# Kernel optimization log

Hardware: AMD Instinct MI355X
Metric: run time of the kernel (lower is better)

The kernel has to match this reference:

```python
import jax, jax.numpy as jnp
import numpy as np

DIM = 1536      # model dim
NH = 12         # num heads
HD = 128        # head dim
F, H, W = 3, 26, 48   # video latent grid (frames, height, width)
S = F * H * W   # sequence length = 3744
B = 1
EPS = 1e-6
C2 = HD // 2    # 64 rotary pairs per head
SPLITS = [C2 - 2 * (C2 // 3), C2 // 3, C2 // 3]  # [22, 21, 21] for (f, h, w)


def _rope_angles():
    """Wan rope_params: concat of per-axis inverse-frequency angle tables, [1024, 64]."""
    def rp(dim):  # returns [1024, dim//2]
        inv = 1.0 / (10000.0 ** (np.arange(0, dim, 2, dtype=np.float64) / dim))
        return np.outer(np.arange(1024, dtype=np.float64), inv)
    a = np.concatenate([rp(HD - 4 * (HD // 6)), rp(2 * (HD // 6)), rp(2 * (HD // 6))], axis=1)
    return jnp.asarray(a, jnp.float32)


def setup_inputs() -> dict:
    key = jax.random.key(0)
    ks = jax.random.split(key, 9)
    std = DIM ** -0.5
    return {
        "x": jax.random.normal(ks[0], (B, S, DIM), jnp.float32),
        "wq": jax.random.normal(ks[1], (DIM, DIM), jnp.float32) * std,
        "bq": jnp.zeros((DIM,), jnp.float32),
        "wk": jax.random.normal(ks[2], (DIM, DIM), jnp.float32) * std,
        "bk": jnp.zeros((DIM,), jnp.float32),
        "wv": jax.random.normal(ks[3], (DIM, DIM), jnp.float32) * std,
        "bv": jnp.zeros((DIM,), jnp.float32),
        "wo": jax.random.normal(ks[4], (DIM, DIM), jnp.float32) * std,
        "bo": jnp.zeros((DIM,), jnp.float32),
        "gq": jnp.ones((DIM,), jnp.float32),   # WanRMSNorm weight for q
        "gk": jnp.ones((DIM,), jnp.float32),   # WanRMSNorm weight for k
        "freqs": _rope_angles(),                # [1024, 64] rotary angles
        "seq_lens": jnp.full((B,), S, jnp.int32),
    }


def _rmsnorm(y, g):
    return y * jax.lax.rsqrt(jnp.mean(jnp.square(y), axis=-1, keepdims=True) + EPS) * g


def _rope_grid(freqs):
    """Build per-position rotary angles [S, C2] from the 3D grid (F,H,W)."""
    af = freqs[:F, :SPLITS[0]]                       # [F, 22]
    ah = freqs[:H, SPLITS[0]:SPLITS[0] + SPLITS[1]]  # [H, 21]
    aw = freqs[:W, SPLITS[0] + SPLITS[1]:]           # [W, 21]
    ang = jnp.concatenate([
        jnp.broadcast_to(af[:, None, None, :], (F, H, W, SPLITS[0])),
        jnp.broadcast_to(ah[None, :, None, :], (F, H, W, SPLITS[1])),
        jnp.broadcast_to(aw[None, None, :, :], (F, H, W, SPLITS[2])),
    ], axis=-1)
    return ang.reshape(S, C2)


def _rope_apply(t, cos, sin):
    # t: [B, S, NH, HD]; pairs (even, odd) rotated by angle.
    tp = t.reshape(B, S, NH, C2, 2)
    xr, xi = tp[..., 0], tp[..., 1]
    yr = xr * cos - xi * sin
    yi = xr * sin + xi * cos
    return jnp.stack([yr, yi], axis=-1).reshape(B, S, NH, HD)


def reference(x, wq, bq, wk, bk, wv, bv, wo, bo, gq, gk, freqs, seq_lens):
    q = _rmsnorm(x @ wq.T + bq, gq).reshape(B, S, NH, HD)
    k = _rmsnorm(x @ wk.T + bk, gk).reshape(B, S, NH, HD)
    v = (x @ wv.T + bv).reshape(B, S, NH, HD)

    ang = _rope_grid(freqs)                    # [S, C2]
    cos = jnp.cos(ang)[None, :, None, :]       # [1, S, 1, C2]
    sin = jnp.sin(ang)[None, :, None, :]
    q = _rope_apply(q, cos, sin)
    k = _rope_apply(k, cos, sin)

    scale = HD ** -0.5
    scores = jnp.einsum('bqhd,bkhd->bhqk', q, k) * scale   # [B, NH, S, S]
    kmask = jnp.arange(S)[None, :] < seq_lens[:, None]     # [B, S]
    scores = jnp.where(kmask[:, None, None, :], scores, jnp.float32(-1e9))
    attn = jax.nn.softmax(scores, axis=-1)
    out = jnp.einsum('bhqk,bkhd->bqhd', attn, v).reshape(B, S, DIM)
    return out @ wo.T + bo
```

## Files before the change

### kernel.cpp

```cpp
#include <hip/hip_runtime.h>
#include <stdint.h>


#define DIM   1536
#define S_TOT 3744
#define NHEAD 12
#define HD    128

using short8 = __attribute__((ext_vector_type(8))) short;
using f32x4  = __attribute__((ext_vector_type(4))) float;
using f32x2  = __attribute__((ext_vector_type(2))) float;

__device__ __forceinline__ unsigned short f2bf(float f) {
  unsigned u = __builtin_bit_cast(unsigned, f);
  u += 0x7fffu + ((u >> 16) & 1u);
  return (unsigned short)(u >> 16);
}

__device__ __forceinline__ void gl_lds16(const void* g, void* l) {
  auto gp = (const __attribute__((address_space(1))) unsigned int*)g;
  auto lp = (__attribute__((address_space(3))) unsigned int*)(uintptr_t)l;
  __builtin_amdgcn_global_load_lds(gp, lp, 16, 0, 0);
}

#define NX4 (S_TOT * DIM / 4)
#define NW4 (DIM * DIM / 4)
__global__ __launch_bounds__(256) void cvt5_kernel(
    const float* __restrict__ x, const float* __restrict__ wq,
    const float* __restrict__ wk, const float* __restrict__ wv,
    const float* __restrict__ wo,
    unsigned short* __restrict__ xb, unsigned short* __restrict__ wqb,
    unsigned short* __restrict__ wkb, unsigned short* __restrict__ wvb,
    unsigned short* __restrict__ wob) {
  int gid = blockIdx.x * 256 + threadIdx.x;
  const float* src; unsigned short* dst; int off;
  if (gid < NX4)                { src = x;  dst = xb;  off = gid; }
  else if (gid < NX4 + NW4)     { src = wq; dst = wqb; off = gid - NX4; }
  else if (gid < NX4 + 2 * NW4) { src = wk; dst = wkb; off = gid - NX4 - NW4; }
  else if (gid < NX4 + 3 * NW4) { src = wv; dst = wvb; off = gid - NX4 - 2 * NW4; }
  else if (gid < NX4 + 4 * NW4) { src = wo; dst = wob; off = gid - NX4 - 3 * NW4; }
  else return;
  float4 v = ((const float4*)src)[off];
  ushort4 o;
  o.x = f2bf(v.x); o.y = f2bf(v.y); o.z = f2bf(v.z); o.w = f2bf(v.w);
  ((ushort4*)dst)[off] = o;
}

__device__ __forceinline__ void gemm_body(const unsigned short* __restrict__ A,
                                          const unsigned short* __restrict__ W,
                                          const float* __restrict__ bias,
                                          float* __restrict__ outF,
                                          unsigned short* __restrict__ outB,
                                          int M, int mode) {
  constexpr int K = DIM, N = DIM;
  __shared__ unsigned short As[128 * 32];
  __shared__ unsigned short Ws[128 * 32];
  int tid = threadIdx.x;
  int w = tid >> 6, lane = tid & 63;
  int wr = w >> 1, wc = w & 1, q4 = lane >> 4, ql = lane & 15;
  int m0 = blockIdx.y * 128, n0 = blockIdx.x * 128;

  f32x4 acc[4][4];
  const f32x4 zero4 = {0.f, 0.f, 0.f, 0.f};
#pragma unroll
  for (int i = 0; i < 4; i++)
#pragma unroll
    for (int j = 0; j < 4; j++) acc[i][j] = zero4;

  for (int k0 = 0; k0 < K; k0 += 32) {
    __syncthreads();
#pragma unroll
    for (int r = 0; r < 2; r++) {
      int idx = r * 256 + tid;
      int row = idx >> 2, ch = idx & 3;
      int am = m0 + row; am = (am < M) ? am : (M - 1);
      gl_lds16(A + (size_t)am * K + k0 + ch * 8, &As[idx * 8]);
      gl_lds16(W + (size_t)(n0 + row) * K + k0 + ch * 8, &Ws[idx * 8]);
    }
    __syncthreads();
    short8 af[4], wf[4];
#pragma unroll
    for (int i = 0; i < 4; i++)
      af[i] = *(const short8*)&As[(wr * 64 + i * 16 + ql) * 32 + q4 * 8];
#pragma unroll
    for (int j = 0; j < 4; j++)
      wf[j] = *(const short8*)&Ws[(wc * 64 + j * 16 + ql) * 32 + q4 * 8];
#pragma unroll
    for (int i = 0; i < 4; i++)
#pragma unroll
      for (int j = 0; j < 4; j++)
        acc[i][j] = __builtin_amdgcn_mfma_f32_16x16x32_bf16(af[i], wf[j], acc[i][j], 0, 0, 0);
  }

  float bb[4];
#pragma unroll
  for (int j = 0; j < 4; j++) bb[j] = bias[n0 + wc * 64 + j * 16 + ql];
#pragma unroll
  for (int i = 0; i < 4; i++) {
#pragma unroll
    for (int rg = 0; rg < 4; rg++) {
      int row = m0 + wr * 64 + i * 16 + q4 * 4 + rg;
      if (row < M) {
#pragma unroll
        for (int j = 0; j < 4; j++) {
          int col = n0 + wc * 64 + j * 16 + ql;
          float v = acc[i][j][rg] + bb[j];
          if (mode == 0) outF[(size_t)row * N + col] = v;
          else           outB[(size_t)row * N + col] = f2bf(v);
        }
      }
    }
  }
}

__global__ __launch_bounds__(256) void gemm_qkv_kernel(
    const unsigned short* __restrict__ xb,
    const unsigned short* __restrict__ wqb, const unsigned short* __restrict__ wkb,
    const unsigned short* __restrict__ wvb,
    const float* __restrict__ bq, const float* __restrict__ bk, const float* __restrict__ bv,
    float* __restrict__ Yq, float* __restrict__ Yk, unsigned short* __restrict__ Vb) {
  int z = blockIdx.z;
  const unsigned short* W = (z == 0) ? wqb : ((z == 1) ? wkb : wvb);
  const float* bias       = (z == 0) ? bq  : ((z == 1) ? bk  : bv);
  float* outF             = (z == 0) ? Yq  : Yk;
  gemm_body(xb, W, bias, outF, Vb, S_TOT, (z == 2) ? 1 : 0);
}

__global__ __launch_bounds__(256) void gemm_out_kernel(
    const unsigned short* __restrict__ AO, const unsigned short* __restrict__ wob,
    const float* __restrict__ bo, float* __restrict__ out) {
  gemm_body(AO, wob, bo, out, nullptr, S_TOT, 0);
}

__global__ __launch_bounds__(256) void normrope_kernel(
    const float* __restrict__ Yq, const float* __restrict__ Yk,
    const float* __restrict__ gq, const float* __restrict__ gk,
    const float* __restrict__ freqs,
    unsigned short* __restrict__ Qb, unsigned short* __restrict__ Kb) {
  int s = blockIdx.x;
  int tid = threadIdx.x;
  int w = tid >> 6, lane = tid & 63;
  const f32x2* yq2 = (const f32x2*)(Yq + (size_t)s * DIM);
  const f32x2* yk2 = (const f32x2*)(Yk + (size_t)s * DIM);
  f32x2 vq[3], vk[3];
  float ssq = 0.f, ssk = 0.f;
#pragma unroll
  for (int r = 0; r < 3; r++) {
    int p = tid + 256 * r;
    vq[r] = yq2[p]; vk[r] = yk2[p];
    ssq += vq[r].x * vq[r].x + vq[r].y * vq[r].y;
    ssk += vk[r].x * vk[r].x + vk[r].y * vk[r].y;
  }
#pragma unroll
  for (int d = 1; d < 64; d <<= 1) {
    ssq += __shfl_xor(ssq, d);
    ssk += __shfl_xor(ssk, d);
  }
  __shared__ float rq[4], rk[4];
  if (lane == 0) { rq[w] = ssq; rk[w] = ssk; }
  __syncthreads();
  float tq = rq[0] + rq[1] + rq[2] + rq[3];
  float tk = rk[0] + rk[1] + rk[2] + rk[3];
  float invq = rsqrtf(tq * (1.f / DIM) + 1e-6f);
  float invk = rsqrtf(tk * (1.f / DIM) + 1e-6f);

  int fi = s / (26 * 48);
  int hi = (s / 48) % 26;
  int wi = s % 48;
#pragma unroll
  for (int r = 0; r < 3; r++) {
    int p = tid + 256 * r;
    int c = p & 63;
    int frow = (c < 22) ? fi : ((c < 43) ? hi : wi);
    float ang = freqs[frow * 64 + c];
    float sn, cs;
    __sincosf(ang, &sn, &cs);
    {
      float a = vq[r].x * invq * gq[2 * p];
      float b = vq[r].y * invq * gq[2 * p + 1];
      ushort2 o; o.x = f2bf(a * cs - b * sn); o.y = f2bf(a * sn + b * cs);
      ((ushort2*)Qb)[(size_t)s * (DIM / 2) + p] = o;
    }
    {
      float a = vk[r].x * invk * gk[2 * p];
      float b = vk[r].y * invk * gk[2 * p + 1];
      ushort2 o; o.x = f2bf(a * cs - b * sn); o.y = f2bf(a * sn + b * cs);
      ((ushort2*)Kb)[(size_t)s * (DIM / 2) + p] = o;
    }
  }
}

__global__ __launch_bounds__(256) void vtrans_kernel(const unsigned short* __restrict__ Vb,
                                                     unsigned short* __restrict__ Vt) {
  int d0 = blockIdx.x * 64, s0 = blockIdx.y * 64;
  __shared__ unsigned short t[64][65];
  int tid = threadIdx.x;
#pragma unroll
  for (int r = 0; r < 4; r++) {
    int idx = r * 256 + tid;
    int sr = idx >> 4, c4 = (idx & 15) * 4;
    ushort4 v; v.x = v.y = v.z = v.w = 0;
    int s = s0 + sr;
    if (s < S_TOT) v = *(const ushort4*)(Vb + (size_t)s * DIM + d0 + c4);
    t[sr][c4 + 0] = v.x; t[sr][c4 + 1] = v.y; t[sr][c4 + 2] = v.z; t[sr][c4 + 3] = v.w;
  }
  __syncthreads();
#pragma unroll
  for (int r = 0; r < 4; r++) {
    int idx = r * 256 + tid;
    int dr = idx >> 4, s4 = (idx & 15) * 4;
    if (s0 + s4 < S_TOT) {
      ushort4 v;
      v.x = t[s4 + 0][dr]; v.y = t[s4 + 1][dr]; v.z = t[s4 + 2][dr]; v.w = t[s4 + 3][dr];
      *(ushort4*)(Vt + (size_t)(d0 + dr) * S_TOT + s0 + s4) = v;
    }
  }
}

__global__ __launch_bounds__(128, 2) void attn_kernel(
    const unsigned short* __restrict__ Qb, const unsigned short* __restrict__ Kb,
    const unsigned short* __restrict__ Vt, unsigned short* __restrict__ AO,
    const int* __restrict__ seq_lens) {
  int h = blockIdx.y;
  int tid = threadIdx.x;
  int w = tid >> 6, lane = tid & 63;
  int q4 = lane >> 4, ql = lane & 15;
  int seqlen = seq_lens[0]; if (seqlen > S_TOT) seqlen = S_TOT;

  __shared__ unsigned short Kl[64 * 128];
  __shared__ unsigned short Vl[128 * 64];
  __shared__ unsigned short Pl[2][32 * 72];
  __shared__ float stat[2][32];

  int q0 = blockIdx.x * 64 + w * 32;
  bool wact = (q0 < S_TOT);

  short8 qf[2][4];
#pragma unroll
  for (int qh = 0; qh < 2; qh++) {
    int qrow = q0 + qh * 16 + ql; if (qrow > S_TOT - 1) qrow = S_TOT - 1;
#pragma unroll
    for (int ks = 0; ks < 4; ks++)
      qf[qh][ks] = *(const short8*)(Qb + (size_t)qrow * DIM + h * HD + ks * 32 + q4 * 8);
  }

  f32x4 o[2][8];
  const f32x4 zero4 = {0.f, 0.f, 0.f, 0.f};
#pragma unroll
  for (int qh = 0; qh < 2; qh++)
#pragma unroll
    for (int nt = 0; nt < 8; nt++) o[qh][nt] = zero4;
  float m_run[2] = {-3.0e38f, -3.0e38f}, l_run[2] = {0.f, 0.f};
  const float sm_scale = 0.08838834764831845f;

  const size_t hoff = (size_t)h * HD;

  for (int kt = 0; kt < (S_TOT + 63) / 64; kt++) {
    int k0 = kt * 64;
    __syncthreads();
    {
      const unsigned short* kseg = Kb + (size_t)k0 * DIM + hoff;
#pragma unroll
      for (int r = 0; r < 8; r++) {
        int idx = r * 128 + tid;
        int row = idx >> 4, c = idx & 15;
        int g = c ^ (row & 15);
        gl_lds16(kseg + (size_t)row * DIM + g * 8, &Kl[idx * 8]);
      }
      int kmax = S_TOT - 8 - k0;
#pragma unroll
      for (int r = 0; r < 8; r++) {
        int idx = r * 128 + tid;
        int row = idx >> 3, c = idx & 7;
        int g = c ^ (row & 7);
        int kc = g * 8; if (kc > kmax) kc = kmax;
        gl_lds16(Vt + (hoff + row) * S_TOT + k0 + kc, &Vl[idx * 8]);
      }
    }
    __syncthreads();
    if (!wact) continue;

    f32x4 st[4][2];
#pragma unroll
    for (int mt = 0; mt < 4; mt++) {
      st[mt][0] = zero4; st[mt][1] = zero4;
#pragma unroll
      for (int ks = 0; ks < 4; ks++) {
        int c = (ks * 4 + q4) ^ ql;
        short8 kf = *(const short8*)&Kl[(mt * 16 + ql) * 128 + c * 8];
        st[mt][0] = __builtin_amdgcn_mfma_f32_16x16x32_bf16(kf, qf[0][ks], st[mt][0], 0, 0, 0);
        st[mt][1] = __builtin_amdgcn_mfma_f32_16x16x32_bf16(kf, qf[1][ks], st[mt][1], 0, 0, 0);
      }
    }

#pragma unroll
    for (int qh = 0; qh < 2; qh++) {
      float sc[16];
      float mloc = -3.0e38f;
#pragma unroll
      for (int mt = 0; mt < 4; mt++)
#pragma unroll
        for (int rg = 0; rg < 4; rg++) {
          int key = k0 + mt * 16 + q4 * 4 + rg;
          float v = st[mt][qh][rg] * sm_scale;
          v = (key < seqlen) ? v : -3.0e38f;
          sc[mt * 4 + rg] = v;
          mloc = fmaxf(mloc, v);
        }
      mloc = fmaxf(mloc, __shfl_xor(mloc, 16));
      mloc = fmaxf(mloc, __shfl_xor(mloc, 32));
      float mnew = fmaxf(m_run[qh], mloc);
      float alpha = __expf(m_run[qh] - mnew);
      m_run[qh] = mnew;
      float lloc = 0.f;
#pragma unroll
      for (int mt = 0; mt < 4; mt++) {
        ushort4 pk;
        float p0 = (k0 + mt * 16 + q4 * 4 + 0 < seqlen) ? __expf(sc[mt * 4 + 0] - mnew) : 0.f;
        float p1 = (k0 + mt * 16 + q4 * 4 + 1 < seqlen) ? __expf(sc[mt * 4 + 1] - mnew) : 0.f;
        float p2 = (k0 + mt * 16 + q4 * 4 + 2 < seqlen) ? __expf(sc[mt * 4 + 2] - mnew) : 0.f;
        float p3 = (k0 + mt * 16 + q4 * 4 + 3 < seqlen) ? __expf(sc[mt * 4 + 3] - mnew) : 0.f;
        lloc += p0 + p1 + p2 + p3;
        pk.x = f2bf(p0); pk.y = f2bf(p1); pk.z = f2bf(p2); pk.w = f2bf(p3);
        *(ushort4*)&Pl[w][(qh * 16 + ql) * 72 + mt * 16 + q4 * 4] = pk;
      }
      lloc += __shfl_xor(lloc, 16);
      lloc += __shfl_xor(lloc, 32);
      l_run[qh] = l_run[qh] * alpha + lloc;
      if (lane < 16) stat[w][qh * 16 + lane] = alpha;
    }

    float ar[2][4];
#pragma unroll
    for (int qh = 0; qh < 2; qh++)
#pragma unroll
      for (int rg = 0; rg < 4; rg++) ar[qh][rg] = stat[w][qh * 16 + q4 * 4 + rg];
#pragma unroll
    for (int qh = 0; qh < 2; qh++)
#pragma unroll
      for (int nt = 0; nt < 8; nt++)
#pragma unroll
        for (int rg = 0; rg < 4; rg++) o[qh][nt][rg] *= ar[qh][rg];

#pragma unroll
    for (int ks2 = 0; ks2 < 2; ks2++) {
      short8 pa0 = *(const short8*)&Pl[w][(0 * 16 + ql) * 72 + ks2 * 32 + q4 * 8];
      short8 pa1 = *(const short8*)&Pl[w][(1 * 16 + ql) * 72 + ks2 * 32 + q4 * 8];
#pragma unroll
      for (int nt = 0; nt < 8; nt++) {
        int c = (ks2 * 4 + q4) ^ (ql & 7);
        short8 vb = *(const short8*)&Vl[(nt * 16 + ql) * 64 + c * 8];
        o[0][nt] = __builtin_amdgcn_mfma_f32_16x16x32_bf16(pa0, vb, o[0][nt], 0, 0, 0);
        o[1][nt] = __builtin_amdgcn_mfma_f32_16x16x32_bf16(pa1, vb, o[1][nt], 0, 0, 0);
      }
    }
  }

  if (wact) {
    if (lane < 16) {
      stat[w][lane]      = 1.0f / l_run[0];
      stat[w][16 + lane] = 1.0f / l_run[1];
    }
#pragma unroll
    for (int qh = 0; qh < 2; qh++) {
#pragma unroll
      for (int rg = 0; rg < 4; rg++) {
        int row = q0 + qh * 16 + q4 * 4 + rg;
        if (row < S_TOT) {
          float il = stat[w][qh * 16 + q4 * 4 + rg];
#pragma unroll
          for (int nt = 0; nt < 8; nt++)
            AO[(size_t)row * DIM + h * HD + nt * 16 + ql] = f2bf(o[qh][nt][rg] * il);
        }
      }
    }
  }
}

extern "C" void kernel_launch(void* const* d_in, const int* in_sizes, int n_in,
                              void* d_out, int out_size, void* d_ws, size_t ws_size,
                              hipStream_t stream) {
  const float* x    = (const float*)d_in[0];
  const float* wq   = (const float*)d_in[1];
  const float* bq   = (const float*)d_in[2];
  const float* wk   = (const float*)d_in[3];
  const float* bk   = (const float*)d_in[4];
  const float* wv   = (const float*)d_in[5];
  const float* bv   = (const float*)d_in[6];
  const float* wo   = (const float*)d_in[7];
  const float* bo   = (const float*)d_in[8];
  const float* gq   = (const float*)d_in[9];
  const float* gk   = (const float*)d_in[10];
  const float* freqs = (const float*)d_in[11];
  const int*   seq  = (const int*)d_in[12];

  char* ws = (char*)d_ws;
  const size_t SZ_X = (size_t)S_TOT * DIM * 2;
  const size_t SZ_W = (size_t)DIM * DIM * 2;
  const size_t SZ_Y = (size_t)S_TOT * DIM * 4;

  unsigned short* xb  = (unsigned short*)(ws);
  unsigned short* wqb = (unsigned short*)(ws + SZ_X);
  unsigned short* wkb = (unsigned short*)(ws + SZ_X + SZ_W);
  unsigned short* wvb = (unsigned short*)(ws + SZ_X + 2 * SZ_W);
  unsigned short* wob = (unsigned short*)(ws + SZ_X + 3 * SZ_W);
  float*          Yq  = (float*)(ws + SZ_X + 4 * SZ_W);
  float*          Yk  = (float*)(ws + SZ_X + 4 * SZ_W + SZ_Y);
  unsigned short* Vb  = (unsigned short*)(ws + SZ_X + 4 * SZ_W + 2 * SZ_Y);
  unsigned short* Qb  = (unsigned short*)(ws + SZ_X + 4 * SZ_W + 2 * SZ_Y + SZ_X);
  unsigned short* Kb  = (unsigned short*)(ws + SZ_X + 4 * SZ_W + 2 * SZ_Y + 2 * SZ_X);
  unsigned short* Vt  = (unsigned short*)(ws + SZ_X + 4 * SZ_W + 2 * SZ_Y + 3 * SZ_X);
  unsigned short* AO  = (unsigned short*)(ws + SZ_X + 4 * SZ_W + 2 * SZ_Y + 4 * SZ_X);

  int total4 = NX4 + 4 * NW4;
  cvt5_kernel<<<dim3((total4 + 255) / 256), 256, 0, stream>>>(
      x, wq, wk, wv, wo, xb, wqb, wkb, wvb, wob);

  gemm_qkv_kernel<<<dim3(DIM / 128, (S_TOT + 127) / 128, 3), 256, 0, stream>>>(
      xb, wqb, wkb, wvb, bq, bk, bv, Yq, Yk, Vb);

  normrope_kernel<<<dim3(S_TOT), 256, 0, stream>>>(Yq, Yk, gq, gk, freqs, Qb, Kb);

  vtrans_kernel<<<dim3(DIM / 64, (S_TOT + 63) / 64), 256, 0, stream>>>(Vb, Vt);

  attn_kernel<<<dim3((S_TOT + 63) / 64, NHEAD), 128, 0, stream>>>(Qb, Kb, Vt, AO, seq);

  gemm_out_kernel<<<dim3(DIM / 128, (S_TOT + 127) / 128), 256, 0, stream>>>(
      AO, wob, bo, (float*)d_out);
}
```

Baseline: 477.5 us.

## Load K/V fragments directly from global memory in single-wave attention blocks

The attention kernel drops the shared-memory staging of K and V tiles and the block-wide barriers. Each 64-thread block now handles 32 queries and reads MFMA operands straight from global memory (relying on L2/L1 for reuse). The softmax scale is folded into Q during norm/rope, and the masking branch is split into unmasked full tiles and masked tail tiles via a template. The alpha and 1/l broadcasts now use shuffles instead of LDS. The change trades the barriers and LDS traffic for more global/cache loads per wave, since K/V are no longer shared between waves.

```diff
diff --git a/kernel.cpp b/kernel.cpp
--- a/kernel.cpp
+++ b/kernel.cpp
@@ -6,6 +6,7 @@
 #define S_TOT 3744
 #define NHEAD 12
 #define HD    128
+#define SM_SCALE 0.08838834764831845f
 
 using short8 = __attribute__((ext_vector_type(8))) short;
 using f32x4  = __attribute__((ext_vector_type(4))) float;
@@ -178,7 +179,9 @@
     {
       float a = vq[r].x * invq * gq[2 * p];
       float b = vq[r].y * invq * gq[2 * p + 1];
-      ushort2 o; o.x = f2bf(a * cs - b * sn); o.y = f2bf(a * sn + b * cs);
+      ushort2 o;
+      o.x = f2bf((a * cs - b * sn) * SM_SCALE);
+      o.y = f2bf((a * sn + b * cs) * SM_SCALE);
       ((ushort2*)Qb)[(size_t)s * (DIM / 2) + p] = o;
     }
     {
@@ -217,28 +220,110 @@
   }
 }
 
-__global__ __launch_bounds__(128, 2) void attn_kernel(
+template <bool MASKED>
+__device__ __forceinline__ void attn_tile(
+    int k0, int seqlen,
+    const unsigned short* __restrict__ Kbase,
+    const unsigned short* __restrict__ Vbase,
+    short8 (&qf)[2][4], f32x4 (&o)[2][8], float (&m_run)[2], float (&l_run)[2],
+    unsigned short* __restrict__ Pl, int q4, int ql) {
+  const f32x4 zero4 = {0.f, 0.f, 0.f, 0.f};
+
+  f32x4 st[4][2];
+#pragma unroll
+  for (int mt = 0; mt < 4; mt++) {
+    int krow = k0 + mt * 16 + ql;
+    if (MASKED) krow = (krow < S_TOT) ? krow : (S_TOT - 1);
+    const unsigned short* kp = Kbase + (size_t)krow * DIM + q4 * 8;
+    st[mt][0] = zero4; st[mt][1] = zero4;
+#pragma unroll
+    for (int ks = 0; ks < 4; ks++) {
+      short8 kf = *(const short8*)(kp + ks * 32);
+      st[mt][0] = __builtin_amdgcn_mfma_f32_16x16x32_bf16(kf, qf[0][ks], st[mt][0], 0, 0, 0);
+      st[mt][1] = __builtin_amdgcn_mfma_f32_16x16x32_bf16(kf, qf[1][ks], st[mt][1], 0, 0, 0);
+    }
+  }
+
+#pragma unroll
+  for (int qh = 0; qh < 2; qh++) {
+    float sc[16];
+    float mloc = -3.0e38f;
+#pragma unroll
+    for (int mt = 0; mt < 4; mt++)
+#pragma unroll
+      for (int rg = 0; rg < 4; rg++) {
+        float v = st[mt][qh][rg];
+        if (MASKED) {
+          int key = k0 + mt * 16 + q4 * 4 + rg;
+          v = (key < seqlen) ? v : -3.0e38f;
+        }
+        sc[mt * 4 + rg] = v;
+        mloc = fmaxf(mloc, v);
+      }
+    mloc = fmaxf(mloc, __shfl_xor(mloc, 16));
+    mloc = fmaxf(mloc, __shfl_xor(mloc, 32));
+    float mnew = fmaxf(m_run[qh], mloc);
+    float alpha = __expf(m_run[qh] - mnew);
+    m_run[qh] = mnew;
+    float lloc = 0.f;
+#pragma unroll
+    for (int mt = 0; mt < 4; mt++) {
+      float p0 = __expf(sc[mt * 4 + 0] - mnew);
+      float p1 = __expf(sc[mt * 4 + 1] - mnew);
+      float p2 = __expf(sc[mt * 4 + 2] - mnew);
+      float p3 = __expf(sc[mt * 4 + 3] - mnew);
+      lloc += p0 + p1 + p2 + p3;
+      ushort4 pk;
+      pk.x = f2bf(p0); pk.y = f2bf(p1); pk.z = f2bf(p2); pk.w = f2bf(p3);
+      *(ushort4*)&Pl[(qh * 16 + ql) * 72 + mt * 16 + q4 * 4] = pk;
+    }
+    lloc += __shfl_xor(lloc, 16);
+    lloc += __shfl_xor(lloc, 32);
+    l_run[qh] = l_run[qh] * alpha + lloc;
+#pragma unroll
+    for (int rg = 0; rg < 4; rg++) {
+      float a = __shfl(alpha, q4 * 4 + rg);
+#pragma unroll
+      for (int nt = 0; nt < 8; nt++) o[qh][nt][rg] *= a;
+    }
+  }
+
+#pragma unroll
+  for (int ks2 = 0; ks2 < 2; ks2++) {
+    short8 pa0 = *(const short8*)&Pl[(0 * 16 + ql) * 72 + ks2 * 32 + q4 * 8];
+    short8 pa1 = *(const short8*)&Pl[(1 * 16 + ql) * 72 + ks2 * 32 + q4 * 8];
+    int kc = k0 + ks2 * 32 + q4 * 8;
+    if (MASKED) kc = (kc < S_TOT - 8) ? kc : (S_TOT - 8);
+#pragma unroll
+    for (int nt = 0; nt < 8; nt++) {
+      short8 vb = *(const short8*)(Vbase + (size_t)(nt * 16 + ql) * S_TOT + kc);
+      o[0][nt] = __builtin_amdgcn_mfma_f32_16x16x32_bf16(pa0, vb, o[0][nt], 0, 0, 0);
+      o[1][nt] = __builtin_amdgcn_mfma_f32_16x16x32_bf16(pa1, vb, o[1][nt], 0, 0, 0);
+    }
+  }
+}
+
+__global__ __launch_bounds__(64, 2) void attn_kernel(
     const unsigned short* __restrict__ Qb, const unsigned short* __restrict__ Kb,
     const unsigned short* __restrict__ Vt, unsigned short* __restrict__ AO,
     const int* __restrict__ seq_lens) {
   int h = blockIdx.y;
-  int tid = threadIdx.x;
-  int w = tid >> 6, lane = tid & 63;
+  int lane = threadIdx.x;
   int q4 = lane >> 4, ql = lane & 15;
-  int seqlen = seq_lens[0]; if (seqlen > S_TOT) seqlen = S_TOT;
-
-  __shared__ unsigned short Kl[64 * 128];
-  __shared__ unsigned short Vl[128 * 64];
-  __shared__ unsigned short Pl[2][32 * 72];
-  __shared__ float stat[2][32];
-
-  int q0 = blockIdx.x * 64 + w * 32;
-  bool wact = (q0 < S_TOT);
+  int seqlen = seq_lens[0];
+  if (seqlen > S_TOT) seqlen = S_TOT;
+  if (seqlen < 1) seqlen = 1;
+
+  __shared__ unsigned short Pl[32 * 72];
+
+  int q0 = blockIdx.x * 32;
+  const unsigned short* Kbase = Kb + (size_t)h * HD;
+  const unsigned short* Vbase = Vt + (size_t)h * HD * S_TOT;
 
   short8 qf[2][4];
 #pragma unroll
   for (int qh = 0; qh < 2; qh++) {
-    int qrow = q0 + qh * 16 + ql; if (qrow > S_TOT - 1) qrow = S_TOT - 1;
+    int qrow = q0 + qh * 16 + ql;
 #pragma unroll
     for (int ks = 0; ks < 4; ks++)
       qf[qh][ks] = *(const short8*)(Qb + (size_t)qrow * DIM + h * HD + ks * 32 + q4 * 8);
@@ -251,128 +336,28 @@
 #pragma unroll
     for (int nt = 0; nt < 8; nt++) o[qh][nt] = zero4;
   float m_run[2] = {-3.0e38f, -3.0e38f}, l_run[2] = {0.f, 0.f};
-  const float sm_scale = 0.08838834764831845f;
-
-  const size_t hoff = (size_t)h * HD;
-
-  for (int kt = 0; kt < (S_TOT + 63) / 64; kt++) {
-    int k0 = kt * 64;
-    __syncthreads();
-    {
-      const unsigned short* kseg = Kb + (size_t)k0 * DIM + hoff;
-#pragma unroll
-      for (int r = 0; r < 8; r++) {
-        int idx = r * 128 + tid;
-        int row = idx >> 4, c = idx & 15;
-        int g = c ^ (row & 15);
-        gl_lds16(kseg + (size_t)row * DIM + g * 8, &Kl[idx * 8]);
-      }
-      int kmax = S_TOT - 8 - k0;
-#pragma unroll
-      for (int r = 0; r < 8; r++) {
-        int idx = r * 128 + tid;
-        int row = idx >> 3, c = idx & 7;
-        int g = c ^ (row & 7);
-        int kc = g * 8; if (kc > kmax) kc = kmax;
-        gl_lds16(Vt + (hoff + row) * S_TOT + k0 + kc, &Vl[idx * 8]);
-      }
-    }
-    __syncthreads();
-    if (!wact) continue;
-
-    f32x4 st[4][2];
-#pragma unroll
-    for (int mt = 0; mt < 4; mt++) {
-      st[mt][0] = zero4; st[mt][1] = zero4;
-#pragma unroll
-      for (int ks = 0; ks < 4; ks++) {
-        int c = (ks * 4 + q4) ^ ql;
-        short8 kf = *(const short8*)&Kl[(mt * 16 + ql) * 128 + c * 8];
-        st[mt][0] = __builtin_amdgcn_mfma_f32_16x16x32_bf16(kf, qf[0][ks], st[mt][0], 0, 0, 0);
-        st[mt][1] = __builtin_amdgcn_mfma_f32_16x16x32_bf16(kf, qf[1][ks], st[mt][1], 0, 0, 0);
-      }
-    }
-
-#pragma unroll
-    for (int qh = 0; qh < 2; qh++) {
-      float sc[16];
-      float mloc = -3.0e38f;
-#pragma unroll
-      for (int mt = 0; mt < 4; mt++)
-#pragma unroll
-        for (int rg = 0; rg < 4; rg++) {
-          int key = k0 + mt * 16 + q4 * 4 + rg;
-          float v = st[mt][qh][rg] * sm_scale;
-          v = (key < seqlen) ? v : -3.0e38f;
-          sc[mt * 4 + rg] = v;
-          mloc = fmaxf(mloc, v);
-        }
-      mloc = fmaxf(mloc, __shfl_xor(mloc, 16));
-      mloc = fmaxf(mloc, __shfl_xor(mloc, 32));
-      float mnew = fmaxf(m_run[qh], mloc);
-      float alpha = __expf(m_run[qh] - mnew);
-      m_run[qh] = mnew;
-      float lloc = 0.f;
-#pragma unroll
-      for (int mt = 0; mt < 4; mt++) {
-        ushort4 pk;
-        float p0 = (k0 + mt * 16 + q4 * 4 + 0 < seqlen) ? __expf(sc[mt * 4 + 0] - mnew) : 0.f;
-        float p1 = (k0 + mt * 16 + q4 * 4 + 1 < seqlen) ? __expf(sc[mt * 4 + 1] - mnew) : 0.f;
-        float p2 = (k0 + mt * 16 + q4 * 4 + 2 < seqlen) ? __expf(sc[mt * 4 + 2] - mnew) : 0.f;
-        float p3 = (k0 + mt * 16 + q4 * 4 + 3 < seqlen) ? __expf(sc[mt * 4 + 3] - mnew) : 0.f;
-        lloc += p0 + p1 + p2 + p3;
-        pk.x = f2bf(p0); pk.y = f2bf(p1); pk.z = f2bf(p2); pk.w = f2bf(p3);
-        *(ushort4*)&Pl[w][(qh * 16 + ql) * 72 + mt * 16 + q4 * 4] = pk;
-      }
-      lloc += __shfl_xor(lloc, 16);
-      lloc += __shfl_xor(lloc, 32);
-      l_run[qh] = l_run[qh] * alpha + lloc;
-      if (lane < 16) stat[w][qh * 16 + lane] = alpha;
-    }
-
-    float ar[2][4];
-#pragma unroll
-    for (int qh = 0; qh < 2; qh++)
-#pragma unroll
-      for (int rg = 0; rg < 4; rg++) ar[qh][rg] = stat[w][qh * 16 + q4 * 4 + rg];
-#pragma unroll
-    for (int qh = 0; qh < 2; qh++)
+
+  int ntiles = (S_TOT + 63) / 64;
+  int nfull = seqlen >> 6;
+  if (nfull > ntiles) nfull = ntiles;
+
+  int kt = 0;
+  for (; kt < nfull; kt++)
+    attn_tile<false>(kt * 64, seqlen, Kbase, Vbase, qf, o, m_run, l_run, Pl, q4, ql);
+  for (; kt < ntiles; kt++)
+    attn_tile<true>(kt * 64, seqlen, Kbase, Vbase, qf, o, m_run, l_run, Pl, q4, ql);
+
+  float linv0 = 1.0f / l_run[0], linv1 = 1.0f / l_run[1];
+#pragma unroll
+  for (int qh = 0; qh < 2; qh++) {
+    float linv = qh ? linv1 : linv0;
+#pragma unroll
+    for (int rg = 0; rg < 4; rg++) {
+      float il = __shfl(linv, q4 * 4 + rg);
+      int row = q0 + qh * 16 + q4 * 4 + rg;
 #pragma unroll
       for (int nt = 0; nt < 8; nt++)
-#pragma unroll
-        for (int rg = 0; rg < 4; rg++) o[qh][nt][rg] *= ar[qh][rg];
-
-#pragma unroll
-    for (int ks2 = 0; ks2 < 2; ks2++) {
-      short8 pa0 = *(const short8*)&Pl[w][(0 * 16 + ql) * 72 + ks2 * 32 + q4 * 8];
-      short8 pa1 = *(const short8*)&Pl[w][(1 * 16 + ql) * 72 + ks2 * 32 + q4 * 8];
-#pragma unroll
-      for (int nt = 0; nt < 8; nt++) {
-        int c = (ks2 * 4 + q4) ^ (ql & 7);
-        short8 vb = *(const short8*)&Vl[(nt * 16 + ql) * 64 + c * 8];
-        o[0][nt] = __builtin_amdgcn_mfma_f32_16x16x32_bf16(pa0, vb, o[0][nt], 0, 0, 0);
-        o[1][nt] = __builtin_amdgcn_mfma_f32_16x16x32_bf16(pa1, vb, o[1][nt], 0, 0, 0);
-      }
-    }
-  }
-
-  if (wact) {
-    if (lane < 16) {
-      stat[w][lane]      = 1.0f / l_run[0];
-      stat[w][16 + lane] = 1.0f / l_run[1];
-    }
-#pragma unroll
-    for (int qh = 0; qh < 2; qh++) {
-#pragma unroll
-      for (int rg = 0; rg < 4; rg++) {
-        int row = q0 + qh * 16 + q4 * 4 + rg;
-        if (row < S_TOT) {
-          float il = stat[w][qh * 16 + q4 * 4 + rg];
-#pragma unroll
-          for (int nt = 0; nt < 8; nt++)
-            AO[(size_t)row * DIM + h * HD + nt * 16 + ql] = f2bf(o[qh][nt][rg] * il);
-        }
-      }
+        AO[(size_t)row * DIM + h * HD + nt * 16 + ql] = f2bf(o[qh][nt][rg] * il);
     }
   }
 }
@@ -423,7 +408,7 @@
 
   vtrans_kernel<<<dim3(DIM / 64, (S_TOT + 63) / 64), 256, 0, stream>>>(Vb, Vt);
 
-  attn_kernel<<<dim3((S_TOT + 63) / 64, NHEAD), 128, 0, stream>>>(Qb, Kb, Vt, AO, seq);
+  attn_kernel<<<dim3(S_TOT / 32, NHEAD), 64, 0, stream>>>(Qb, Kb, Vt, AO, seq);
 
   gemm_out_kernel<<<dim3(DIM / 128, (S_TOT + 127) / 128), 256, 0, stream>>>(
       AO, wob, bo, (float*)d_out);
```

Result: slower. 533.0 us (+11.6%).

## Split attention over KV halves with combine kernel, load V directly to registers

Applied to the files above, without the earlier changes.

Splits the key range of attention into two halves along a new grid z-dimension, writing unnormalized partial outputs and per-row max/sum stats, then merges them in a new combine kernel (flash-decoding style split-K). This doubles the block count (59x12 to 59x12x2) to improve occupancy on the many CUs. It also folds the softmax scale into Q during norm/rope, skips masking work on full tiles, loads V fragments straight from global memory into registers instead of through LDS, and replaces the LDS alpha broadcast with shuffles. The cost is extra fp32 partial-output traffic, reuse of the Yq/Yk buffers, and an extra kernel launch.

```diff
diff --git a/kernel.cpp b/kernel.cpp
--- a/kernel.cpp
+++ b/kernel.cpp
@@ -6,6 +6,8 @@
 #define S_TOT 3744
 #define NHEAD 12
 #define HD    128
+#define SNH   (S_TOT * NHEAD)
+#define SM_SCALE 0.08838834764831845f
 
 using short8 = __attribute__((ext_vector_type(8))) short;
 using f32x4  = __attribute__((ext_vector_type(4))) float;
@@ -178,7 +180,9 @@
     {
       float a = vq[r].x * invq * gq[2 * p];
       float b = vq[r].y * invq * gq[2 * p + 1];
-      ushort2 o; o.x = f2bf(a * cs - b * sn); o.y = f2bf(a * sn + b * cs);
+      ushort2 o;
+      o.x = f2bf((a * cs - b * sn) * SM_SCALE);
+      o.y = f2bf((a * sn + b * cs) * SM_SCALE);
       ((ushort2*)Qb)[(size_t)s * (DIM / 2) + p] = o;
     }
     {
@@ -219,22 +223,26 @@
 
 __global__ __launch_bounds__(128, 2) void attn_kernel(
     const unsigned short* __restrict__ Qb, const unsigned short* __restrict__ Kb,
-    const unsigned short* __restrict__ Vt, unsigned short* __restrict__ AO,
+    const unsigned short* __restrict__ Vt,
+    float* __restrict__ Op0, float* __restrict__ Op1, float* __restrict__ Ml,
     const int* __restrict__ seq_lens) {
-  int h = blockIdx.y;
+  int h = blockIdx.y, z = blockIdx.z;
   int tid = threadIdx.x;
   int w = tid >> 6, lane = tid & 63;
   int q4 = lane >> 4, ql = lane & 15;
-  int seqlen = seq_lens[0]; if (seqlen > S_TOT) seqlen = S_TOT;
+  int seqlen = seq_lens[0];
+  if (seqlen > S_TOT) seqlen = S_TOT;
+  if (seqlen < 1) seqlen = 1;
 
   __shared__ unsigned short Kl[64 * 128];
-  __shared__ unsigned short Vl[128 * 64];
   __shared__ unsigned short Pl[2][32 * 72];
-  __shared__ float stat[2][32];
 
   int q0 = blockIdx.x * 64 + w * 32;
   bool wact = (q0 < S_TOT);
 
+  const unsigned short* Kbase = Kb + (size_t)h * HD;
+  const unsigned short* Vbase = Vt + (size_t)h * HD * S_TOT;
+
   short8 qf[2][4];
 #pragma unroll
   for (int qh = 0; qh < 2; qh++) {
@@ -251,32 +259,29 @@
 #pragma unroll
     for (int nt = 0; nt < 8; nt++) o[qh][nt] = zero4;
   float m_run[2] = {-3.0e38f, -3.0e38f}, l_run[2] = {0.f, 0.f};
-  const float sm_scale = 0.08838834764831845f;
-
-  const size_t hoff = (size_t)h * HD;
-
-  for (int kt = 0; kt < (S_TOT + 63) / 64; kt++) {
+
+  int t0 = z ? 30 : 0, t1 = z ? 59 : 30;
+  for (int kt = t0; kt < t1; kt++) {
     int k0 = kt * 64;
+    bool masked = (k0 + 64 > seqlen);
     __syncthreads();
-    {
-      const unsigned short* kseg = Kb + (size_t)k0 * DIM + hoff;
-#pragma unroll
-      for (int r = 0; r < 8; r++) {
-        int idx = r * 128 + tid;
-        int row = idx >> 4, c = idx & 15;
-        int g = c ^ (row & 15);
-        gl_lds16(kseg + (size_t)row * DIM + g * 8, &Kl[idx * 8]);
-      }
-      int kmax = S_TOT - 8 - k0;
-#pragma unroll
-      for (int r = 0; r < 8; r++) {
-        int idx = r * 128 + tid;
-        int row = idx >> 3, c = idx & 7;
-        int g = c ^ (row & 7);
-        int kc = g * 8; if (kc > kmax) kc = kmax;
-        gl_lds16(Vt + (hoff + row) * S_TOT + k0 + kc, &Vl[idx * 8]);
-      }
-    }
+#pragma unroll
+    for (int r = 0; r < 8; r++) {
+      int idx = r * 128 + tid;
+      int row = idx >> 4, c = idx & 15;
+      int g = c ^ (row & 15);
+      gl_lds16(Kbase + (size_t)(k0 + row) * DIM + g * 8, &Kl[idx * 8]);
+    }
+    short8 vb[2][8];
+#pragma unroll
+    for (int ks2 = 0; ks2 < 2; ks2++) {
+      int kc = k0 + ks2 * 32 + q4 * 8;
+      if (masked && kc > S_TOT - 8) kc = S_TOT - 8;
+#pragma unroll
+      for (int nt = 0; nt < 8; nt++)
+        vb[ks2][nt] = *(const short8*)(Vbase + (size_t)(nt * 16 + ql) * S_TOT + kc);
+    }
+    __builtin_amdgcn_sched_barrier(0);
     __syncthreads();
     if (!wact) continue;
 
@@ -301,9 +306,11 @@
       for (int mt = 0; mt < 4; mt++)
 #pragma unroll
         for (int rg = 0; rg < 4; rg++) {
-          int key = k0 + mt * 16 + q4 * 4 + rg;
-          float v = st[mt][qh][rg] * sm_scale;
-          v = (key < seqlen) ? v : -3.0e38f;
+          float v = st[mt][qh][rg];
+          if (masked) {
+            int key = k0 + mt * 16 + q4 * 4 + rg;
+            v = (key < seqlen) ? v : -3.0e38f;
+          }
           sc[mt * 4 + rg] = v;
           mloc = fmaxf(mloc, v);
         }
@@ -315,32 +322,34 @@
       float lloc = 0.f;
 #pragma unroll
       for (int mt = 0; mt < 4; mt++) {
+        float p0, p1, p2, p3;
+        if (masked) {
+          int kb = k0 + mt * 16 + q4 * 4;
+          p0 = (kb + 0 < seqlen) ? __expf(sc[mt * 4 + 0] - mnew) : 0.f;
+          p1 = (kb + 1 < seqlen) ? __expf(sc[mt * 4 + 1] - mnew) : 0.f;
+          p2 = (kb + 2 < seqlen) ? __expf(sc[mt * 4 + 2] - mnew) : 0.f;
+          p3 = (kb + 3 < seqlen) ? __expf(sc[mt * 4 + 3] - mnew) : 0.f;
+        } else {
+          p0 = __expf(sc[mt * 4 + 0] - mnew);
+          p1 = __expf(sc[mt * 4 + 1] - mnew);
+          p2 = __expf(sc[mt * 4 + 2] - mnew);
+          p3 = __expf(sc[mt * 4 + 3] - mnew);
+        }
+        lloc += p0 + p1 + p2 + p3;
         ushort4 pk;
-        float p0 = (k0 + mt * 16 + q4 * 4 + 0 < seqlen) ? __expf(sc[mt * 4 + 0] - mnew) : 0.f;
-        float p1 = (k0 + mt * 16 + q4 * 4 + 1 < seqlen) ? __expf(sc[mt * 4 + 1] - mnew) : 0.f;
-        float p2 = (k0 + mt * 16 + q4 * 4 + 2 < seqlen) ? __expf(sc[mt * 4 + 2] - mnew) : 0.f;
-        float p3 = (k0 + mt * 16 + q4 * 4 + 3 < seqlen) ? __expf(sc[mt * 4 + 3] - mnew) : 0.f;
-        lloc += p0 + p1 + p2 + p3;
         pk.x = f2bf(p0); pk.y = f2bf(p1); pk.z = f2bf(p2); pk.w = f2bf(p3);
         *(ushort4*)&Pl[w][(qh * 16 + ql) * 72 + mt * 16 + q4 * 4] = pk;
       }
       lloc += __shfl_xor(lloc, 16);
       lloc += __shfl_xor(lloc, 32);
       l_run[qh] = l_run[qh] * alpha + lloc;
-      if (lane < 16) stat[w][qh * 16 + lane] = alpha;
-    }
-
-    float ar[2][4];
-#pragma unroll
-    for (int qh = 0; qh < 2; qh++)
-#pragma unroll
-      for (int rg = 0; rg < 4; rg++) ar[qh][rg] = stat[w][qh * 16 + q4 * 4 + rg];
-#pragma unroll
-    for (int qh = 0; qh < 2; qh++)
-#pragma unroll
-      for (int nt = 0; nt < 8; nt++)
-#pragma unroll
-        for (int rg = 0; rg < 4; rg++) o[qh][nt][rg] *= ar[qh][rg];
+#pragma unroll
+      for (int rg = 0; rg < 4; rg++) {
+        float a = __shfl(alpha, q4 * 4 + rg);
+#pragma unroll
+        for (int nt = 0; nt < 8; nt++) o[qh][nt][rg] *= a;
+      }
+    }
 
 #pragma unroll
     for (int ks2 = 0; ks2 < 2; ks2++) {
@@ -348,33 +357,65 @@
       short8 pa1 = *(const short8*)&Pl[w][(1 * 16 + ql) * 72 + ks2 * 32 + q4 * 8];
 #pragma unroll
       for (int nt = 0; nt < 8; nt++) {
-        int c = (ks2 * 4 + q4) ^ (ql & 7);
-        short8 vb = *(const short8*)&Vl[(nt * 16 + ql) * 64 + c * 8];
-        o[0][nt] = __builtin_amdgcn_mfma_f32_16x16x32_bf16(pa0, vb, o[0][nt], 0, 0, 0);
-        o[1][nt] = __builtin_amdgcn_mfma_f32_16x16x32_bf16(pa1, vb, o[1][nt], 0, 0, 0);
+        o[0][nt] = __builtin_amdgcn_mfma_f32_16x16x32_bf16(pa0, vb[ks2][nt], o[0][nt], 0, 0, 0);
+        o[1][nt] = __builtin_amdgcn_mfma_f32_16x16x32_bf16(pa1, vb[ks2][nt], o[1][nt], 0, 0, 0);
       }
     }
   }
 
   if (wact) {
-    if (lane < 16) {
-      stat[w][lane]      = 1.0f / l_run[0];
-      stat[w][16 + lane] = 1.0f / l_run[1];
-    }
+    float* Op = z ? Op1 : Op0;
 #pragma unroll
     for (int qh = 0; qh < 2; qh++) {
 #pragma unroll
       for (int rg = 0; rg < 4; rg++) {
         int row = q0 + qh * 16 + q4 * 4 + rg;
         if (row < S_TOT) {
-          float il = stat[w][qh * 16 + q4 * 4 + rg];
 #pragma unroll
           for (int nt = 0; nt < 8; nt++)
-            AO[(size_t)row * DIM + h * HD + nt * 16 + ql] = f2bf(o[qh][nt][rg] * il);
+            Op[(size_t)row * DIM + h * HD + nt * 16 + ql] = o[qh][nt][rg];
         }
       }
     }
-  }
+    if (lane < 16) {
+      int row0 = q0 + lane;
+      if (row0 < S_TOT) {
+        Ml[(2 * z + 0) * SNH + row0 * NHEAD + h] = m_run[0];
+        Ml[(2 * z + 1) * SNH + row0 * NHEAD + h] = l_run[0];
+      }
+      int row1 = q0 + 16 + lane;
+      if (row1 < S_TOT) {
+        Ml[(2 * z + 0) * SNH + row1 * NHEAD + h] = m_run[1];
+        Ml[(2 * z + 1) * SNH + row1 * NHEAD + h] = l_run[1];
+      }
+    }
+  }
+}
+
+__global__ __launch_bounds__(256) void combine_kernel(
+    const float* __restrict__ Op0, const float* __restrict__ Op1,
+    const float* __restrict__ Ml, unsigned short* __restrict__ AO) {
+  int idx = blockIdx.x * 256 + threadIdx.x;
+  if (idx >= S_TOT * DIM / 4) return;
+  int s = idx / (DIM / 4);
+  int rem = idx - s * (DIM / 4);
+  int h = rem / (HD / 4);
+  float m0 = Ml[0 * SNH + s * NHEAD + h];
+  float l0 = Ml[1 * SNH + s * NHEAD + h];
+  float m1 = Ml[2 * SNH + s * NHEAD + h];
+  float l1 = Ml[3 * SNH + s * NHEAD + h];
+  float m = fmaxf(m0, m1);
+  float w0 = __expf(m0 - m), w1 = __expf(m1 - m);
+  float inv = 1.0f / (l0 * w0 + l1 * w1);
+  w0 *= inv; w1 *= inv;
+  float4 a = ((const float4*)Op0)[idx];
+  float4 b = ((const float4*)Op1)[idx];
+  ushort4 ov;
+  ov.x = f2bf(a.x * w0 + b.x * w1);
+  ov.y = f2bf(a.y * w0 + b.y * w1);
+  ov.z = f2bf(a.z * w0 + b.z * w1);
+  ov.w = f2bf(a.w * w0 + b.w * w1);
+  ((ushort4*)AO)[idx] = ov;
 }
 
 extern "C" void kernel_launch(void* const* d_in, const int* in_sizes, int n_in,
@@ -411,6 +452,7 @@
   unsigned short* Kb  = (unsigned short*)(ws + SZ_X + 4 * SZ_W + 2 * SZ_Y + 2 * SZ_X);
   unsigned short* Vt  = (unsigned short*)(ws + SZ_X + 4 * SZ_W + 2 * SZ_Y + 3 * SZ_X);
   unsigned short* AO  = (unsigned short*)(ws + SZ_X + 4 * SZ_W + 2 * SZ_Y + 4 * SZ_X);
+  float*          Ml  = (float*)(ws + SZ_X + 4 * SZ_W + 2 * SZ_Y + 5 * SZ_X);
 
   int total4 = NX4 + 4 * NW4;
   cvt5_kernel<<<dim3((total4 + 255) / 256), 256, 0, stream>>>(
@@ -423,7 +465,11 @@
 
   vtrans_kernel<<<dim3(DIM / 64, (S_TOT + 63) / 64), 256, 0, stream>>>(Vb, Vt);
 
-  attn_kernel<<<dim3((S_TOT + 63) / 64, NHEAD), 128, 0, stream>>>(Qb, Kb, Vt, AO, seq);
+  attn_kernel<<<dim3((S_TOT + 63) / 64, NHEAD, 2), 128, 0, stream>>>(
+      Qb, Kb, Vt, Yq, Yk, Ml, seq);
+
+  combine_kernel<<<dim3((S_TOT * DIM / 4 + 255) / 256), 256, 0, stream>>>(
+      Yq, Yk, Ml, AO);
 
   gemm_out_kernel<<<dim3(DIM / 128, (S_TOT + 127) / 128), 256, 0, stream>>>(
       AO, wob, bo, (float*)d_out);
```

Measured after the change: 491.9 us. 3.0% more time.
